# Performance work log

Hardware: AMD Instinct MI355X
Metric: run time of the kernel (lower is better)

Reference implementation:

```python
import jax, jax.numpy as jnp
import numpy as np

D_MODEL = 2048
N_HEADS = 16
HEAD_DIM = D_MODEL // N_HEADS  # 128
MAX_T = 2048
ROPE_BASE = 10000.0


def _rope_tables(head_dim, max_t, base):
    inv = 1.0 / (base ** (np.arange(0, head_dim, 2, dtype=np.float32) / head_dim))
    t = np.arange(max_t, dtype=np.float32)
    fr = np.outer(t, inv)  # (T, head_dim//2)
    return jnp.asarray(np.cos(fr)), jnp.asarray(np.sin(fr))


def setup_inputs() -> dict:
    key = jax.random.key(0)
    k1, k2, k3 = jax.random.split(key, 3)
    B, T = 2, 2048
    x = jax.random.normal(k1, (B, T, D_MODEL), dtype=jnp.float32)
    Wqkv = jax.random.normal(k2, (3 * D_MODEL, D_MODEL), dtype=jnp.float32) * 0.02
    Wout = jax.random.normal(k3, (D_MODEL, D_MODEL), dtype=jnp.float32) * 0.02
    cos, sin = _rope_tables(HEAD_DIM, MAX_T, ROPE_BASE)
    rope_mask = jnp.arange(N_HEADS) < (N_HEADS // 2)  # first 8 heads RoPE, rest NoPE
    return {"x": x, "Wqkv": Wqkv, "Wout": Wout, "cos": cos, "sin": sin, "rope_mask": rope_mask}


def _apply_rope(t, cos, sin):
    # t: (B,H,T,hd); pairs are consecutive elements (x0,x1),(x2,x3),...
    B, H, T, hd = t.shape
    tr = t.reshape(B, H, T, hd // 2, 2)
    c = cos[:T][None, None, :, :]
    s = sin[:T][None, None, :, :]
    re = tr[..., 0] * c - tr[..., 1] * s
    im = tr[..., 0] * s + tr[..., 1] * c
    return jnp.stack([re, im], axis=-1).reshape(B, H, T, hd)


def reference(x, Wqkv, Wout, cos, sin, rope_mask):
    B, T, D = x.shape
    H = rope_mask.shape[0]
    hd = D // H
    qkv = x @ Wqkv.T  # (B,T,3D)
    q, k, v = jnp.split(qkv, 3, axis=-1)
    def heads(a):
        return a.reshape(B, T, H, hd).transpose(0, 2, 1, 3)  # (B,H,T,hd)
    q, k, v = heads(q), heads(k), heads(v)
    m = rope_mask[None, :, None, None]  # broadcast over (B,H,T,hd)
    q = jnp.where(m, _apply_rope(q, cos, sin), q)
    k = jnp.where(m, _apply_rope(k, cos, sin), k)
    scale = 1.0 / jnp.sqrt(jnp.asarray(hd, dtype=q.dtype))
    scores = jnp.einsum('bhtd,bhsd->bhts', q, k) * scale
    causal = jnp.tril(jnp.ones((T, T), dtype=bool))
    scores = jnp.where(causal[None, None], scores, jnp.asarray(-jnp.inf, dtype=scores.dtype))
    p = jax.nn.softmax(scores, axis=-1)
    out = jnp.einsum('bhts,bhsd->bhtd', p, v)
    out = out.transpose(0, 2, 1, 3).reshape(B, T, D)
    return out @ Wout.T
```

## Files before the change

### kernel.cpp

```cpp
#include <hip/hip_runtime.h>
#include <stdint.h>

typedef unsigned short u16;
typedef __attribute__((ext_vector_type(8))) short short8;
typedef __attribute__((ext_vector_type(4))) short s16x4;
typedef __attribute__((ext_vector_type(4))) float f32x4;
typedef __attribute__((ext_vector_type(16))) float f32x16;

__device__ __forceinline__ u16 f2bf(float f) {
  uint32_t x = __float_as_uint(f);
  x += 0x7fff + ((x >> 16) & 1);
  return (u16)(x >> 16);
}
__device__ __forceinline__ float bf2f(u16 u) {
  return __uint_as_float(((uint32_t)u) << 16);
}
__device__ __forceinline__ f32x4 mfma16(short8 a, short8 b, f32x4 c) {
  return __builtin_amdgcn_mfma_f32_16x16x32_bf16(a, b, c, 0, 0, 0);
}
__device__ __forceinline__ f32x16 mfma32(short8 a, short8 b, f32x16 c) {
  return __builtin_amdgcn_mfma_f32_32x32x16_bf16(a, b, c, 0, 0, 0);
}
__device__ __forceinline__ f32x4 mfma16k16(s16x4 a, s16x4 b, f32x4 c) {
  return __builtin_amdgcn_mfma_f32_16x16x16bf16_1k(a, b, c, 0, 0, 0);
}
__device__ __forceinline__ void gld16(const u16* g, u16* l) {
  __builtin_amdgcn_global_load_lds(
      (const __attribute__((address_space(1))) unsigned int*)g,
      (__attribute__((address_space(3))) unsigned int*)l, 16, 0, 0);
}
__device__ __forceinline__ float exp2a(float x) {
  float r;
  asm("v_exp_f32 %0, %1" : "=v"(r) : "v"(x));
  return r;
}

#define WAIT_VM(n) asm volatile("s_waitcnt vmcnt(" #n ")" ::: "memory")

__global__ __launch_bounds__(256) void cvt_all(const float* __restrict__ x,
                                               const float* __restrict__ wqkv,
                                               const float* __restrict__ wout,
                                               u16* __restrict__ xb,
                                               u16* __restrict__ wqkvb,
                                               u16* __restrict__ woutb) {
  long i = ((long)blockIdx.x * 256 + threadIdx.x) * 8;
  const float* s;
  u16* d;
  long off;
  if (i < 8388608) {
    s = x; d = xb; off = i;
  } else if (i < 20971520) {
    s = wqkv; d = wqkvb; off = i - 8388608;
  } else {
    s = wout; d = woutb; off = i - 20971520;
  }
  f32x4 a = *(const f32x4*)(s + off);
  f32x4 b = *(const f32x4*)(s + off + 4);
  short8 o;
#pragma unroll
  for (int j = 0; j < 4; j++) {
    o[j] = (short)f2bf(a[j]);
    o[j + 4] = (short)f2bf(b[j]);
  }
  *(short8*)(d + off) = o;
}

__global__ __launch_bounds__(512, 2) void gemm_qkv(const u16* __restrict__ A,
                                                   const u16* __restrict__ Bw,
                                                   u16* __restrict__ q3) {
  __shared__ __align__(16) u16 SA[32768];
  __shared__ __align__(16) u16 SB[32768];
  const int id = blockIdx.x;
  const int swz = (id & 7) * 48 + (id >> 3);
  const int by = swz & 15, bx = swz >> 4;
  const int m0 = by * 256, n0 = bx * 256;
  const int t = threadIdx.x, w = t >> 6, lane = t & 63;
  const int quad = lane >> 4, l15 = lane & 15;
  const int wm = w >> 2, wn = w & 3;
  const int rS = t >> 2, pS = t & 3;
  const int cS = (pS - (rS >> 1)) & 3;
  const size_t arow = (size_t)(m0 + rS) * 2048 + cS * 8;
  const size_t brow = (size_t)(n0 + rS) * 2048 + cS * 8;

  f32x4 acc[8][4] = {};
  const int pq = ((quad + (l15 >> 1)) & 3) * 8;

#define STAGE_PAIR(KT)                                                        \
  {                                                                           \
    const u16* ga_ = A + arow + (size_t)(KT) * 32;                            \
    u16* la_ = SA + ((KT) & 3) * 8192 + t * 8;                                \
    gld16(ga_, la_);                                                          \
    gld16(ga_ + (size_t)128 * 2048, la_ + 4096);                              \
    const u16* gb_ = Bw + brow + (size_t)(KT) * 32;                           \
    u16* lb_ = SB + ((KT) & 3) * 8192 + t * 8;                                \
    gld16(gb_, lb_);                                                          \
    gld16(gb_ + (size_t)128 * 2048, lb_ + 4096);                              \
  }

#define TILE(RING, TAU, DO_STAGE, WAIT)                                       \
  {                                                                           \
    const u16* Sa_ = SA + (RING) * 8192;                                      \
    const u16* Sb_ = SB + (RING) * 8192;                                      \
    if (DO_STAGE) STAGE_PAIR((TAU) + 3);                                      \
    short8 af[4], af2[4], bfr[4];                                             \
    _Pragma("unroll") for (int i = 0; i < 4; i++)                             \
        af[i] = *(const short8*)&Sa_[(wm * 128 + i * 16 + l15) * 32 + pq];    \
    _Pragma("unroll") for (int n = 0; n < 4; n++)                             \
        bfr[n] = *(const short8*)&Sb_[(wn * 64 + n * 16 + l15) * 32 + pq];    \
    _Pragma("unroll") for (int i = 0; i < 4; i++)                             \
        af2[i] = *(const short8*)&Sa_[(wm * 128 + 64 + i * 16 + l15) * 32 + pq]; \
    __builtin_amdgcn_s_setprio(1);                                            \
    _Pragma("unroll") for (int mi = 0; mi < 4; mi++)                          \
      _Pragma("unroll") for (int ni = 0; ni < 4; ni++)                        \
          acc[mi][ni] = mfma16(af[mi], bfr[ni], acc[mi][ni]);                 \
    _Pragma("unroll") for (int mi = 0; mi < 4; mi++)                          \
      _Pragma("unroll") for (int ni = 0; ni < 4; ni++)                        \
          acc[4 + mi][ni] = mfma16(af2[mi], bfr[ni], acc[4 + mi][ni]);        \
    __builtin_amdgcn_s_setprio(0);                                            \
    WAIT;                                                                     \
    __builtin_amdgcn_s_barrier();                                             \
  }

  STAGE_PAIR(0);
  STAGE_PAIR(1);
  STAGE_PAIR(2);
  WAIT_VM(8);
  __builtin_amdgcn_s_barrier();

#pragma unroll 1
  for (int kt = 0; kt < 60; kt += 4) {
    TILE(0, kt + 0, true, WAIT_VM(8));
    TILE(1, kt + 1, true, WAIT_VM(8));
    TILE(2, kt + 2, true, WAIT_VM(8));
    TILE(3, kt + 3, true, WAIT_VM(8));
  }
  TILE(0, 60, true, WAIT_VM(8));
  TILE(1, 61, false, WAIT_VM(4));
  TILE(2, 62, false, WAIT_VM(0));
  TILE(3, 63, false, (void)0);
#undef TILE
#undef STAGE_PAIR

  const int which = n0 >> 11;
  const int bb = m0 >> 11, tt0 = m0 & 2047;
  if (which == 2) {
    u16* vbase = q3 + 16777216;
#pragma unroll
    for (int ni = 0; ni < 4; ni++) {
      const int gcol = (n0 & 2047) + wn * 64 + ni * 16 + l15;
      const int hh = gcol >> 7, di = gcol & 127;
      u16* vb = vbase + ((size_t)(bb * 16 + hh) * 128 + di) * 2048;
#pragma unroll
      for (int mi = 0; mi < 8; mi++) {
        const int tloc = tt0 + wm * 128 + mi * 16 + quad * 4;
        s16x4 st;
#pragma unroll
        for (int r = 0; r < 4; r++) st[r] = (short)f2bf(acc[mi][ni][r]);
        *(s16x4*)(vb + tloc) = st;
      }
    }
  } else {
    const float sc = (which == 0) ? 0.1275174f : 1.0f;
    u16* base = q3 + (size_t)which * 8388608;
#pragma unroll
    for (int ni = 0; ni < 4; ni++) {
      const int gcol = (n0 & 2047) + wn * 64 + ni * 16 + l15;
      const int hh = gcol >> 7, di = gcol & 127;
      u16* qb = base + ((size_t)(bb * 16 + hh) * 2048) * 128 + di;
#pragma unroll
      for (int mi = 0; mi < 8; mi++) {
        const int tloc = tt0 + wm * 128 + mi * 16 + quad * 4;
#pragma unroll
        for (int r = 0; r < 4; r++)
          qb[(size_t)(tloc + r) * 128] = f2bf(acc[mi][ni][r] * sc);
      }
    }
  }
}

template <int EPI>
__global__ __launch_bounds__(256) void gemm_bt(const u16* __restrict__ A,
                                               const u16* __restrict__ B,
                                               int K, void* __restrict__ Cv, int N) {
  __shared__ __align__(16) u16 SMEM[8448];
  u16* As = SMEM;
  u16* Bs = SMEM + 4096;
  const int m0 = blockIdx.y * 128, n0 = blockIdx.x * 128;
  const int t = threadIdx.x, w = t >> 6, lane = t & 63;
  const int l31 = lane & 31, half = lane >> 5;
  const int rb = (w >> 1) * 64, cb = (w & 1) * 64;
  f32x16 acc[2][2] = {};
  const int rowS = w * 16 + (lane >> 2);
  const int cS = ((lane & 3) - (rowS >> 1)) & 3;
  const u16* ag = A + (size_t)(m0 + rowS) * K + cS * 8;
  const u16* bg = B + (size_t)(n0 + rowS) * K + cS * 8;
  u16* al = As + w * 512 + lane * 8;
  u16* bl = Bs + w * 512 + lane * 8;
  const size_t rowskip = (size_t)64 * K;
  const int p0 = ((0 * 2 + half + (l31 >> 1)) & 3) * 8;
  const int p1 = ((1 * 2 + half + (l31 >> 1)) & 3) * 8;
  for (int k0 = 0; k0 < K; k0 += 32) {
    __syncthreads();
    gld16(ag, al);
    gld16(ag + rowskip, al + 2048);
    gld16(bg, bl);
    gld16(bg + rowskip, bl + 2048);
    ag += 32;
    bg += 32;
    __syncthreads();
    short8 af[2][2], bfr[2][2];
#pragma unroll
    for (int mi = 0; mi < 2; mi++) {
      af[mi][0] = *(const short8*)&As[(rb + mi * 32 + l31) * 32 + p0];
      af[mi][1] = *(const short8*)&As[(rb + mi * 32 + l31) * 32 + p1];
    }
#pragma unroll
    for (int ni = 0; ni < 2; ni++) {
      bfr[ni][0] = *(const short8*)&Bs[(cb + ni * 32 + l31) * 32 + p0];
      bfr[ni][1] = *(const short8*)&Bs[(cb + ni * 32 + l31) * 32 + p1];
    }
#pragma unroll
    for (int kh = 0; kh < 2; kh++)
#pragma unroll
      for (int mi = 0; mi < 2; mi++)
#pragma unroll
        for (int ni = 0; ni < 2; ni++)
          acc[mi][ni] = mfma32(af[mi][kh], bfr[ni][kh], acc[mi][ni]);
  }

  if (EPI == 0) {
    const int which = n0 >> 11;
    const int hh = (n0 & 2047) >> 7;
    const int bb = m0 >> 11, tt0 = m0 & 2047;
    u16* q3 = (u16*)Cv;
    if (which == 2) {
      u16* vbase = q3 + 16777216 + ((size_t)(bb * 16 + hh) * 128) * 2048;
#pragma unroll
      for (int mi = 0; mi < 2; mi++)
#pragma unroll
        for (int ni = 0; ni < 2; ni++) {
          int di = cb + ni * 32 + l31;
          int trow = tt0 + rb + mi * 32 + half * 4;
#pragma unroll
          for (int rg2 = 0; rg2 < 4; rg2++) {
            s16x4 st;
#pragma unroll
            for (int j = 0; j < 4; j++) st[j] = (short)f2bf(acc[mi][ni][rg2 * 4 + j]);
            *(s16x4*)(vbase + (size_t)di * 2048 + trow + rg2 * 8) = st;
          }
        }
    } else {
      const float sc = (which == 0) ? 0.1275174f : 1.0f;
      u16* base = q3 + (size_t)which * 8388608 + ((size_t)(bb * 16 + hh) * 2048) * 128;
#pragma unroll
      for (int mi = 0; mi < 2; mi++)
#pragma unroll
        for (int ni = 0; ni < 2; ni++) {
          int di = cb + ni * 32 + l31;
          int trow = tt0 + rb + mi * 32 + half * 4;
#pragma unroll
          for (int reg = 0; reg < 16; reg++) {
            int tt = trow + (reg & 3) + 8 * (reg >> 2);
            base[(size_t)tt * 128 + di] = f2bf(acc[mi][ni][reg] * sc);
          }
        }
    }
  } else {
    float* Es = (float*)SMEM;
    float* C = (float*)Cv;
#pragma unroll
    for (int r = 0; r < 4; r++) {
      __syncthreads();
      if ((w >> 1) == (r >> 1)) {
        const int mi = r & 1;
#pragma unroll
        for (int ni = 0; ni < 2; ni++) {
          int col = cb + ni * 32 + l31;
#pragma unroll
          for (int reg = 0; reg < 16; reg++) {
            int lrow = (reg & 3) + 8 * (reg >> 2) + half * 4;
            Es[lrow * 132 + col] = acc[mi][ni][reg];
          }
        }
      }
      __syncthreads();
#pragma unroll
      for (int it = 0; it < 4; it++) {
        int idx = it * 256 + t;
        int row = idx >> 5, ch = idx & 31;
        f32x4 vv = *(const f32x4*)&Es[row * 132 + ch * 4];
        *(f32x4*)&C[(size_t)(m0 + r * 32 + row) * N + n0 + ch * 4] = vv;
      }
    }
  }
}

__global__ __launch_bounds__(256) void rope_k(u16* __restrict__ q, u16* __restrict__ k,
                                              const float* __restrict__ cosT,
                                              const float* __restrict__ sinT) {
  int t = threadIdx.x;
  int row = blockIdx.x * 4 + (t >> 6);
  int i = t & 63;
  int b = row >> 14;
  int h = (row >> 11) & 7;
  int tp = row & 2047;
  size_t base = ((size_t)((b * 16 + h) * 2048 + tp)) * 128 + 2 * i;
  float c = cosT[tp * 64 + i], s = sinT[tp * 64 + i];
  {
    uint32_t u = *(uint32_t*)(q + base);
    float x0 = bf2f((u16)(u & 0xffff)), x1 = bf2f((u16)(u >> 16));
    float re = x0 * c - x1 * s, im = x0 * s + x1 * c;
    *(uint32_t*)(q + base) = (uint32_t)f2bf(re) | ((uint32_t)f2bf(im) << 16);
  }
  {
    uint32_t u = *(uint32_t*)(k + base);
    float x0 = bf2f((u16)(u & 0xffff)), x1 = bf2f((u16)(u >> 16));
    float re = x0 * c - x1 * s, im = x0 * s + x1 * c;
    *(uint32_t*)(k + base) = (uint32_t)f2bf(re) | ((uint32_t)f2bf(im) << 16);
  }
}

__global__ __launch_bounds__(256, 2) void attn_k(const u16* __restrict__ qh,
                                                 const u16* __restrict__ kh,
                                                 const u16* __restrict__ vTh,
                                                 u16* __restrict__ attno) {
  __shared__ __align__(16) u16 Ks[8192];
  __shared__ __align__(16) u16 Vt[8192];
  const int i = blockIdx.x;
  const int jj = i & 255, half = i >> 8;
  const int bh = jj >> 3, t8 = jj & 7;
  const int qt = half ? (15 - t8) : t8;
  const int q0 = qt * 128;
  const int t = threadIdx.x, w = t >> 6, lane = t & 63;
  const int quad = lane >> 4, l15 = lane & 15;
  const size_t bhoff = (size_t)bh * 262144;

  short8 qb[2][4];
  {
    const u16* qp = qh + bhoff + (size_t)(q0 + w * 32 + l15) * 128 + quad * 8;
#pragma unroll
    for (int qq = 0; qq < 2; qq++)
#pragma unroll
      for (int ks = 0; ks < 4; ks++)
        qb[qq][ks] = *(const short8*)(qp + qq * 2048 + ks * 32);
  }
  f32x4 of[2][8] = {};
  float mst[2] = {-1e30f, -1e30f}, lst[2] = {0.f, 0.f};
  const int nkt = 2 * qt + 2;
  const int wq0 = q0 + w * 32;

  for (int kt = 0; kt < nkt; kt++) {
    const int k0 = kt * 64;
    __syncthreads();
    {
#pragma unroll
      for (int it = 0; it < 4; it++) {
        int L = it * 256 + t;
        int key = L >> 4, c = L & 15;
        gld16(kh + bhoff + (size_t)(k0 + key) * 128 + ((c ^ (key & 15)) * 8),
              Ks + (size_t)L * 8);
      }
#pragma unroll
      for (int it = 0; it < 4; it++) {
        int L = it * 256 + t;
        int d = L >> 3, c = L & 7;
        gld16(vTh + bhoff + (size_t)d * 2048 + k0 + ((c ^ (d & 7)) * 8),
              Vt + (size_t)L * 8);
      }
    }
    __syncthreads();
    if (k0 <= wq0 + 31) {
      f32x4 sacc[2][4];
#pragma unroll
      for (int qq = 0; qq < 2; qq++)
#pragma unroll
        for (int kk = 0; kk < 4; kk++) sacc[qq][kk] = (f32x4){0.f, 0.f, 0.f, 0.f};
#pragma unroll
      for (int kk = 0; kk < 4; kk++) {
        short8 kf[4];
#pragma unroll
        for (int ks = 0; ks < 4; ks++)
          kf[ks] = *(const short8*)&Ks[(kk * 16 + l15) * 128 + ((ks * 4 + quad) ^ l15) * 8];
#pragma unroll
        for (int qq = 0; qq < 2; qq++)
#pragma unroll
          for (int ks = 0; ks < 4; ks++)
            sacc[qq][kk] = mfma16(kf[ks], qb[qq][ks], sacc[qq][kk]);
      }
      const bool needmask = (k0 + 63 > wq0);
      s16x4 pf[2][4];
      float alpha[2];
#pragma unroll
      for (int qq = 0; qq < 2; qq++) {
        const int qg = wq0 + qq * 16 + l15;
        if (needmask) {
#pragma unroll
          for (int kk = 0; kk < 4; kk++)
#pragma unroll
            for (int rg = 0; rg < 4; rg++)
              if (k0 + kk * 16 + quad * 4 + rg > qg) sacc[qq][kk][rg] = -1e30f;
        }
        float pm = -1e30f;
#pragma unroll
        for (int kk = 0; kk < 4; kk++)
#pragma unroll
          for (int rg = 0; rg < 4; rg++) pm = fmaxf(pm, sacc[qq][kk][rg]);
        pm = fmaxf(pm, __shfl_xor(pm, 16));
        pm = fmaxf(pm, __shfl_xor(pm, 32));
        float mnew = fmaxf(mst[qq], pm);
        alpha[qq] = exp2a(mst[qq] - mnew);
        mst[qq] = mnew;
        float ps = 0.f;
#pragma unroll
        for (int kk = 0; kk < 4; kk++) {
          float e0 = exp2a(sacc[qq][kk][0] - mnew);
          float e1 = exp2a(sacc[qq][kk][1] - mnew);
          float e2 = exp2a(sacc[qq][kk][2] - mnew);
          float e3 = exp2a(sacc[qq][kk][3] - mnew);
          ps += (e0 + e1) + (e2 + e3);
          pf[qq][kk][0] = (short)f2bf(e0);
          pf[qq][kk][1] = (short)f2bf(e1);
          pf[qq][kk][2] = (short)f2bf(e2);
          pf[qq][kk][3] = (short)f2bf(e3);
        }
        ps += __shfl_xor(ps, 16);
        ps += __shfl_xor(ps, 32);
        lst[qq] = lst[qq] * alpha[qq] + ps;
      }
#pragma unroll
      for (int qq = 0; qq < 2; qq++) {
        if (!__all(alpha[qq] == 1.0f)) {
          float a = alpha[qq];
#pragma unroll
          for (int df = 0; df < 8; df++) of[qq][df] *= a;
        }
      }
#pragma unroll
      for (int df = 0; df < 8; df++) {
        s16x4 vf[4];
#pragma unroll
        for (int kk = 0; kk < 4; kk++)
          vf[kk] = *(const s16x4*)&Vt[(df * 16 + l15) * 64 +
                                      ((kk * 2 + (quad >> 1)) ^ (l15 & 7)) * 8 +
                                      (quad & 1) * 4];
#pragma unroll
        for (int qq = 0; qq < 2; qq++)
#pragma unroll
          for (int kk = 0; kk < 4; kk++)
            of[qq][df] = mfma16k16(vf[kk], pf[qq][kk], of[qq][df]);
      }
    }
  }
  const int b = bh >> 4, h = bh & 15;
#pragma unroll
  for (int qq = 0; qq < 2; qq++) {
    float linv = 1.0f / lst[qq];
    const size_t row = (size_t)(b * 2048 + q0 + w * 32 + qq * 16 + l15);
#pragma unroll
    for (int df = 0; df < 8; df++) {
      s16x4 o;
#pragma unroll
      for (int rg = 0; rg < 4; rg++) o[rg] = (short)f2bf(of[qq][df][rg] * linv);
      *(s16x4*)(attno + row * 2048 + h * 128 + df * 16 + quad * 4) = o;
    }
  }
}

extern "C" void kernel_launch(void* const* d_in, const int* in_sizes, int n_in,
                              void* d_out, int out_size, void* d_ws, size_t ws_size,
                              hipStream_t stream) {
  const float* x = (const float*)d_in[0];
  const float* Wqkv = (const float*)d_in[1];
  const float* Wout = (const float*)d_in[2];
  const float* cosT = (const float*)d_in[3];
  const float* sinT = (const float*)d_in[4];
  float* out = (float*)d_out;
  char* ws = (char*)d_ws;
  u16* qkvh = (u16*)(ws + 0);
  u16* woutb = (u16*)(ws + 50331648);
  u16* xb = (u16*)(ws + 58720256);
  u16* wqkvb = (u16*)(ws + 75497472);
  u16* attno = wqkvb;

  cvt_all<<<12288, 256, 0, stream>>>(x, Wqkv, Wout, xb, wqkvb, woutb);
  gemm_qkv<<<384, 512, 0, stream>>>(xb, wqkvb, qkvh);
  rope_k<<<8192, 256, 0, stream>>>(qkvh, qkvh + 8388608, cosT, sinT);
  attn_k<<<512, 256, 0, stream>>>(qkvh, qkvh + 8388608, qkvh + 16777216, attno);
  gemm_bt<1><<<dim3(16, 32), 256, 0, stream>>>(attno, woutb, 2048, (void*)out, 2048);
}
```

Baseline: 408.8 us.

## Software-pipeline LDS fragment loads with MFMA in QKV GEMM main loop

Splits each K-tile's 8x4 MFMA block into four 4x2 quadrants and interleaves the LDS fragment reads between them. The low A/B fragments of the next ring slot are prefetched into double-buffered registers during the current tile. The aim is to hide LDS read latency behind matrix-core work, at the cost of more live registers. It also tightens the global-load wait from two stages in flight to one, which may expose more global memory latency.

```diff
diff --git a/kernel.cpp b/kernel.cpp
--- a/kernel.cpp
+++ b/kernel.cpp
@@ -97,47 +97,75 @@
     gld16(gb_ + (size_t)128 * 2048, lb_ + 4096);                              \
   }
 
-#define TILE(RING, TAU, DO_STAGE, WAIT)                                       \
-  {                                                                           \
-    const u16* Sa_ = SA + (RING) * 8192;                                      \
-    const u16* Sb_ = SB + (RING) * 8192;                                      \
-    if (DO_STAGE) STAGE_PAIR((TAU) + 3);                                      \
-    short8 af[4], af2[4], bfr[4];                                             \
-    _Pragma("unroll") for (int i = 0; i < 4; i++)                             \
-        af[i] = *(const short8*)&Sa_[(wm * 128 + i * 16 + l15) * 32 + pq];    \
-    _Pragma("unroll") for (int n = 0; n < 4; n++)                             \
-        bfr[n] = *(const short8*)&Sb_[(wn * 64 + n * 16 + l15) * 32 + pq];    \
-    _Pragma("unroll") for (int i = 0; i < 4; i++)                             \
-        af2[i] = *(const short8*)&Sa_[(wm * 128 + 64 + i * 16 + l15) * 32 + pq]; \
-    __builtin_amdgcn_s_setprio(1);                                            \
-    _Pragma("unroll") for (int mi = 0; mi < 4; mi++)                          \
-      _Pragma("unroll") for (int ni = 0; ni < 4; ni++)                        \
-          acc[mi][ni] = mfma16(af[mi], bfr[ni], acc[mi][ni]);                 \
-    _Pragma("unroll") for (int mi = 0; mi < 4; mi++)                          \
-      _Pragma("unroll") for (int ni = 0; ni < 4; ni++)                        \
-          acc[4 + mi][ni] = mfma16(af2[mi], bfr[ni], acc[4 + mi][ni]);        \
-    __builtin_amdgcn_s_setprio(0);                                            \
-    WAIT;                                                                     \
-    __builtin_amdgcn_s_barrier();                                             \
+  short8 aflo0[4], bflo0[2], aflo1[4], bflo1[2];
+
+#define TILE(RC, RN, TAU, ALO_C, BLO_C, ALO_N, BLO_N, DO_STAGE, DO_PREF, WAIT)   \
+  {                                                                              \
+    const u16* Sa_ = SA + (RC) * 8192;                                           \
+    const u16* Sb_ = SB + (RC) * 8192;                                           \
+    const u16* San_ = SA + (RN) * 8192;                                          \
+    const u16* Sbn_ = SB + (RN) * 8192;                                          \
+    if (DO_STAGE) STAGE_PAIR((TAU) + 3);                                         \
+    short8 afhi[4], bfhi[2];                                                     \
+    _Pragma("unroll") for (int i = 0; i < 4; i++)                                \
+        afhi[i] = *(const short8*)&Sa_[(wm * 128 + 64 + i * 16 + l15) * 32 + pq];\
+    __builtin_amdgcn_s_setprio(1);                                               \
+    _Pragma("unroll") for (int mi = 0; mi < 4; mi++)                             \
+      _Pragma("unroll") for (int ni = 0; ni < 2; ni++)                           \
+          acc[mi][ni] = mfma16(ALO_C[mi], BLO_C[ni], acc[mi][ni]);               \
+    __builtin_amdgcn_s_setprio(0);                                               \
+    _Pragma("unroll") for (int n = 0; n < 2; n++)                                \
+        bfhi[n] = *(const short8*)&Sb_[(wn * 64 + (n + 2) * 16 + l15) * 32 + pq];\
+    __builtin_amdgcn_s_setprio(1);                                               \
+    _Pragma("unroll") for (int mi = 0; mi < 4; mi++)                             \
+      _Pragma("unroll") for (int ni = 0; ni < 2; ni++)                           \
+          acc[4 + mi][ni] = mfma16(afhi[mi], BLO_C[ni], acc[4 + mi][ni]);        \
+    __builtin_amdgcn_s_setprio(0);                                               \
+    if (DO_PREF) {                                                               \
+      _Pragma("unroll") for (int i = 0; i < 4; i++)                              \
+          ALO_N[i] = *(const short8*)&San_[(wm * 128 + i * 16 + l15) * 32 + pq]; \
+    }                                                                            \
+    __builtin_amdgcn_s_setprio(1);                                               \
+    _Pragma("unroll") for (int mi = 0; mi < 4; mi++)                             \
+      _Pragma("unroll") for (int ni = 0; ni < 2; ni++)                           \
+          acc[4 + mi][2 + ni] = mfma16(afhi[mi], bfhi[ni], acc[4 + mi][2 + ni]); \
+    __builtin_amdgcn_s_setprio(0);                                               \
+    if (DO_PREF) {                                                               \
+      _Pragma("unroll") for (int n = 0; n < 2; n++)                              \
+          BLO_N[n] = *(const short8*)&Sbn_[(wn * 64 + n * 16 + l15) * 32 + pq];  \
+    }                                                                            \
+    __builtin_amdgcn_s_setprio(1);                                               \
+    _Pragma("unroll") for (int mi = 0; mi < 4; mi++)                             \
+      _Pragma("unroll") for (int ni = 0; ni < 2; ni++)                           \
+          acc[mi][2 + ni] = mfma16(ALO_C[mi], bfhi[ni], acc[mi][2 + ni]);        \
+    __builtin_amdgcn_s_setprio(0);                                               \
+    WAIT;                                                                        \
+    __builtin_amdgcn_s_barrier();                                                \
   }
 
   STAGE_PAIR(0);
   STAGE_PAIR(1);
   STAGE_PAIR(2);
-  WAIT_VM(8);
+  WAIT_VM(4);
   __builtin_amdgcn_s_barrier();
+#pragma unroll
+  for (int i = 0; i < 4; i++)
+    aflo0[i] = *(const short8*)&SA[(wm * 128 + i * 16 + l15) * 32 + pq];
+#pragma unroll
+  for (int n = 0; n < 2; n++)
+    bflo0[n] = *(const short8*)&SB[(wn * 64 + n * 16 + l15) * 32 + pq];
 
 #pragma unroll 1
   for (int kt = 0; kt < 60; kt += 4) {
-    TILE(0, kt + 0, true, WAIT_VM(8));
-    TILE(1, kt + 1, true, WAIT_VM(8));
-    TILE(2, kt + 2, true, WAIT_VM(8));
-    TILE(3, kt + 3, true, WAIT_VM(8));
-  }
-  TILE(0, 60, true, WAIT_VM(8));
-  TILE(1, 61, false, WAIT_VM(4));
-  TILE(2, 62, false, WAIT_VM(0));
-  TILE(3, 63, false, (void)0);
+    TILE(0, 1, kt + 0, aflo0, bflo0, aflo1, bflo1, 1, 1, WAIT_VM(4));
+    TILE(1, 2, kt + 1, aflo1, bflo1, aflo0, bflo0, 1, 1, WAIT_VM(4));
+    TILE(2, 3, kt + 2, aflo0, bflo0, aflo1, bflo1, 1, 1, WAIT_VM(4));
+    TILE(3, 0, kt + 3, aflo1, bflo1, aflo0, bflo0, 1, 1, WAIT_VM(4));
+  }
+  TILE(0, 1, 60, aflo0, bflo0, aflo1, bflo1, 1, 1, WAIT_VM(4));
+  TILE(1, 2, 61, aflo1, bflo1, aflo0, bflo0, 0, 1, WAIT_VM(0));
+  TILE(2, 3, 62, aflo0, bflo0, aflo1, bflo1, 0, 1, (void)0);
+  TILE(3, 0, 63, aflo1, bflo1, aflo0, bflo0, 0, 0, (void)0);
 #undef TILE
 #undef STAGE_PAIR
 
@@ -152,7 +180,8 @@
       u16* vb = vbase + ((size_t)(bb * 16 + hh) * 128 + di) * 2048;
 #pragma unroll
       for (int mi = 0; mi < 8; mi++) {
-        const int tloc = tt0 + wm * 128 + mi * 16 + quad * 4;
+        const int mrow = (mi < 4) ? mi * 16 : 64 + (mi - 4) * 16;
+        const int tloc = tt0 + wm * 128 + mrow + quad * 4;
         s16x4 st;
 #pragma unroll
         for (int r = 0; r < 4; r++) st[r] = (short)f2bf(acc[mi][ni][r]);
@@ -169,7 +198,8 @@
       u16* qb = base + ((size_t)(bb * 16 + hh) * 2048) * 128 + di;
 #pragma unroll
       for (int mi = 0; mi < 8; mi++) {
-        const int tloc = tt0 + wm * 128 + mi * 16 + quad * 4;
+        const int mrow = (mi < 4) ? mi * 16 : 64 + (mi - 4) * 16;
+        const int tloc = tt0 + wm * 128 + mrow + quad * 4;
 #pragma unroll
         for (int r = 0; r < 4; r++)
           qb[(size_t)(tloc + r) * 128] = f2bf(acc[mi][ni][r] * sc);
```

New measurement: 407.4 us. No clear change (-0.3%).

## Shrink QKV GEMM tile to 128x256 with 3-stage pipeline for higher occupancy

Applied to the files above, without the earlier changes.

The QKV projection GEMM tile drops from 256x256 to 128x256, doubling the grid to 768 blocks. The LDS ring goes from 4 stages to 3, and launch bounds now ask for 4 blocks per CU. Each warp keeps half as many accumulators, so it can raise occupancy and give the 256 CUs more blocks to balance. In exchange, each K-step reuses loaded data less, the B tile is loaded twice as often, and the shallower pipeline hides less latency.

```diff
diff --git a/kernel.cpp b/kernel.cpp
--- a/kernel.cpp
+++ b/kernel.cpp
@@ -65,81 +65,72 @@
   *(short8*)(d + off) = o;
 }
 
-__global__ __launch_bounds__(512, 2) void gemm_qkv(const u16* __restrict__ A,
+__global__ __launch_bounds__(512, 4) void gemm_qkv(const u16* __restrict__ A,
                                                    const u16* __restrict__ Bw,
                                                    u16* __restrict__ q3) {
-  __shared__ __align__(16) u16 SA[32768];
-  __shared__ __align__(16) u16 SB[32768];
+  __shared__ __align__(16) u16 SA[12288];
+  __shared__ __align__(16) u16 SB[24576];
   const int id = blockIdx.x;
-  const int swz = (id & 7) * 48 + (id >> 3);
-  const int by = swz & 15, bx = swz >> 4;
-  const int m0 = by * 256, n0 = bx * 256;
+  const int swz = (id & 7) * 96 + (id >> 3);
+  const int by = swz & 31, bx = swz >> 5;
+  const int m0 = by * 128, n0 = bx * 256;
   const int t = threadIdx.x, w = t >> 6, lane = t & 63;
   const int quad = lane >> 4, l15 = lane & 15;
   const int wm = w >> 2, wn = w & 3;
   const int rS = t >> 2, pS = t & 3;
   const int cS = (pS - (rS >> 1)) & 3;
-  const size_t arow = (size_t)(m0 + rS) * 2048 + cS * 8;
-  const size_t brow = (size_t)(n0 + rS) * 2048 + cS * 8;
-
-  f32x4 acc[8][4] = {};
+  const size_t arowA = (size_t)(m0 + rS) * 2048 + cS * 8;
+  const size_t arowB = (size_t)(n0 + rS) * 2048 + cS * 8;
+
+  f32x4 acc[4][4] = {};
   const int pq = ((quad + (l15 >> 1)) & 3) * 8;
 
-#define STAGE_PAIR(KT)                                                        \
+#define STAGE(KT, RS_)                                   \
+  {                                                      \
+    const u16* ga_ = A + arowA + (size_t)(KT) * 32;      \
+    gld16(ga_, SA + (RS_)*4096 + t * 8);                 \
+    const u16* gb_ = Bw + arowB + (size_t)(KT) * 32;     \
+    u16* lb_ = SB + (RS_)*8192 + t * 8;                  \
+    gld16(gb_, lb_);                                     \
+    gld16(gb_ + (size_t)128 * 2048, lb_ + 4096);         \
+  }
+
+#define TILE(RC, RSS, TAU, DO_STAGE, WAIT)                                    \
   {                                                                           \
-    const u16* ga_ = A + arow + (size_t)(KT) * 32;                            \
-    u16* la_ = SA + ((KT) & 3) * 8192 + t * 8;                                \
-    gld16(ga_, la_);                                                          \
-    gld16(ga_ + (size_t)128 * 2048, la_ + 4096);                              \
-    const u16* gb_ = Bw + brow + (size_t)(KT) * 32;                           \
-    u16* lb_ = SB + ((KT) & 3) * 8192 + t * 8;                                \
-    gld16(gb_, lb_);                                                          \
-    gld16(gb_ + (size_t)128 * 2048, lb_ + 4096);                              \
-  }
-
-#define TILE(RING, TAU, DO_STAGE, WAIT)                                       \
-  {                                                                           \
-    const u16* Sa_ = SA + (RING) * 8192;                                      \
-    const u16* Sb_ = SB + (RING) * 8192;                                      \
-    if (DO_STAGE) STAGE_PAIR((TAU) + 3);                                      \
-    short8 af[4], af2[4], bfr[4];                                             \
+    const u16* Sa_ = SA + (RC)*4096;                                          \
+    const u16* Sb_ = SB + (RC)*8192;                                          \
+    if (DO_STAGE) STAGE((TAU) + 2, RSS);                                      \
+    short8 af[4], bf[4];                                                      \
     _Pragma("unroll") for (int i = 0; i < 4; i++)                             \
-        af[i] = *(const short8*)&Sa_[(wm * 128 + i * 16 + l15) * 32 + pq];    \
+        af[i] = *(const short8*)&Sa_[(wm * 64 + i * 16 + l15) * 32 + pq];     \
     _Pragma("unroll") for (int n = 0; n < 4; n++)                             \
-        bfr[n] = *(const short8*)&Sb_[(wn * 64 + n * 16 + l15) * 32 + pq];    \
-    _Pragma("unroll") for (int i = 0; i < 4; i++)                             \
-        af2[i] = *(const short8*)&Sa_[(wm * 128 + 64 + i * 16 + l15) * 32 + pq]; \
+        bf[n] = *(const short8*)&Sb_[(wn * 64 + n * 16 + l15) * 32 + pq];     \
     __builtin_amdgcn_s_setprio(1);                                            \
     _Pragma("unroll") for (int mi = 0; mi < 4; mi++)                          \
       _Pragma("unroll") for (int ni = 0; ni < 4; ni++)                        \
-          acc[mi][ni] = mfma16(af[mi], bfr[ni], acc[mi][ni]);                 \
-    _Pragma("unroll") for (int mi = 0; mi < 4; mi++)                          \
-      _Pragma("unroll") for (int ni = 0; ni < 4; ni++)                        \
-          acc[4 + mi][ni] = mfma16(af2[mi], bfr[ni], acc[4 + mi][ni]);        \
+          acc[mi][ni] = mfma16(af[mi], bf[ni], acc[mi][ni]);                  \
     __builtin_amdgcn_s_setprio(0);                                            \
     WAIT;                                                                     \
     __builtin_amdgcn_s_barrier();                                             \
   }
 
-  STAGE_PAIR(0);
-  STAGE_PAIR(1);
-  STAGE_PAIR(2);
-  WAIT_VM(8);
+  STAGE(0, 0);
+  STAGE(1, 1);
+  WAIT_VM(3);
   __builtin_amdgcn_s_barrier();
 
 #pragma unroll 1
-  for (int kt = 0; kt < 60; kt += 4) {
-    TILE(0, kt + 0, true, WAIT_VM(8));
-    TILE(1, kt + 1, true, WAIT_VM(8));
-    TILE(2, kt + 2, true, WAIT_VM(8));
-    TILE(3, kt + 3, true, WAIT_VM(8));
-  }
-  TILE(0, 60, true, WAIT_VM(8));
-  TILE(1, 61, false, WAIT_VM(4));
-  TILE(2, 62, false, WAIT_VM(0));
-  TILE(3, 63, false, (void)0);
+  for (int kt = 0; kt < 60; kt += 3) {
+    TILE(0, 2, kt + 0, 1, WAIT_VM(3));
+    TILE(1, 0, kt + 1, 1, WAIT_VM(3));
+    TILE(2, 1, kt + 2, 1, WAIT_VM(3));
+  }
+  TILE(0, 2, 60, 1, WAIT_VM(3));
+  TILE(1, 0, 61, 1, WAIT_VM(3));
+  TILE(2, 1, 62, 0, WAIT_VM(0));
+  TILE(0, 2, 63, 0, (void)0);
 #undef TILE
-#undef STAGE_PAIR
+#undef STAGE
 
   const int which = n0 >> 11;
   const int bb = m0 >> 11, tt0 = m0 & 2047;
@@ -151,8 +142,8 @@
       const int hh = gcol >> 7, di = gcol & 127;
       u16* vb = vbase + ((size_t)(bb * 16 + hh) * 128 + di) * 2048;
 #pragma unroll
-      for (int mi = 0; mi < 8; mi++) {
-        const int tloc = tt0 + wm * 128 + mi * 16 + quad * 4;
+      for (int mi = 0; mi < 4; mi++) {
+        const int tloc = tt0 + wm * 64 + mi * 16 + quad * 4;
         s16x4 st;
 #pragma unroll
         for (int r = 0; r < 4; r++) st[r] = (short)f2bf(acc[mi][ni][r]);
@@ -168,8 +159,8 @@
       const int hh = gcol >> 7, di = gcol & 127;
       u16* qb = base + ((size_t)(bb * 16 + hh) * 2048) * 128 + di;
 #pragma unroll
-      for (int mi = 0; mi < 8; mi++) {
-        const int tloc = tt0 + wm * 128 + mi * 16 + quad * 4;
+      for (int mi = 0; mi < 4; mi++) {
+        const int tloc = tt0 + wm * 64 + mi * 16 + quad * 4;
 #pragma unroll
         for (int r = 0; r < 4; r++)
           qb[(size_t)(tloc + r) * 128] = f2bf(acc[mi][ni][r] * sc);
@@ -483,7 +474,7 @@
   u16* attno = wqkvb;
 
   cvt_all<<<12288, 256, 0, stream>>>(x, Wqkv, Wout, xb, wqkvb, woutb);
-  gemm_qkv<<<384, 512, 0, stream>>>(xb, wqkvb, qkvh);
+  gemm_qkv<<<768, 512, 0, stream>>>(xb, wqkvb, qkvh);
   rope_k<<<8192, 256, 0, stream>>>(qkvh, qkvh + 8388608, cosT, sinT);
   attn_k<<<512, 256, 0, stream>>>(qkvh, qkvh + 8388608, qkvh + 16777216, attno);
   gemm_bt<1><<<dim3(16, 32), 256, 0, stream>>>(attno, woutb, 2048, (void*)out, 2048);
```

After: 395.2 us. -3.3%, faster.
